# Kernel optimization log

Measured on AMD Instinct MI355X. Metric: run time of the kernel, lower is better.

## Reference

```python
import jax, jax.numpy as jnp
import numpy as np

DEPTH = 4
HEADS = 12
DIM_HEAD = 64
DIM = 768
INNER = HEADS * DIM_HEAD
MLP = 3072
K = 64
KM_ITERS = 10
B, N = 32, 196


def setup_inputs() -> dict:
    key = jax.random.key(0)
    ks = jax.random.split(key, 10)
    s = 0.02
    inp = {}
    inp["x"] = jax.random.normal(ks[0], (B, N, DIM), jnp.float32)
    inp["ln1_w"] = jnp.ones((DEPTH, DIM), jnp.float32)
    inp["ln1_b"] = jnp.zeros((DEPTH, DIM), jnp.float32)
    inp["wq"] = jax.random.normal(ks[1], (DEPTH, DIM, INNER), jnp.float32) * s
    inp["wk"] = jax.random.normal(ks[2], (DEPTH, DIM, INNER), jnp.float32) * s
    inp["wv"] = jax.random.normal(ks[3], (DEPTH, DIM, INNER), jnp.float32) * s
    inp["wo"] = jax.random.normal(ks[4], (DEPTH, INNER, DIM), jnp.float32) * s
    inp["bo"] = jnp.zeros((DEPTH, DIM), jnp.float32)
    inp["ln2_w"] = jnp.ones((DEPTH, DIM), jnp.float32)
    inp["ln2_b"] = jnp.zeros((DEPTH, DIM), jnp.float32)
    inp["w1"] = jax.random.normal(ks[5], (DEPTH, DIM, MLP), jnp.float32) * s
    inp["b1"] = jnp.zeros((DEPTH, MLP), jnp.float32)
    inp["w2"] = jax.random.normal(ks[6], (DEPTH, MLP, DIM), jnp.float32) * s
    inp["b2"] = jnp.zeros((DEPTH, DIM), jnp.float32)
    inp["ct_w"] = jax.random.normal(ks[7], (DIM, DIM), jnp.float32) * s
    inp["ct_b"] = jnp.zeros((DIM,), jnp.float32)
    return inp


def _layernorm(x, w, b, eps=1e-5):
    m = x.mean(-1, keepdims=True)
    v = jnp.mean((x - m) ** 2, -1, keepdims=True)
    return (x - m) * jax.lax.rsqrt(v + eps) * w + b


def _assign(points, centers):
    # squared distances [N, K] via expansion; argmin per point
    d = (jnp.sum(points ** 2, -1, keepdims=True)
         - 2.0 * points @ centers.T
         + jnp.sum(centers ** 2, -1))
    return jnp.argmin(d, axis=-1)


def _kmeans(points, k=K, iters=KM_ITERS):
    # Lloyd's algorithm, deterministic init = first k points
    centers0 = points[:k]

    def step(i, centers):
        labels = _assign(points, centers)
        sums = jax.ops.segment_sum(points, labels, num_segments=k)
        cnts = jax.ops.segment_sum(jnp.ones((points.shape[0],), points.dtype), labels, num_segments=k)
        new_c = sums / jnp.maximum(cnts, 1.0)[:, None]
        return jnp.where(cnts[:, None] > 0, new_c, centers)

    centers = jax.lax.fori_loop(0, iters, step, centers0)
    labels = _assign(points, centers)
    return centers, labels


def reference(x, ln1_w, ln1_b, wq, wk, wv, wo, bo, ln2_w, ln2_b, w1, b1, w2, b2, ct_w, ct_b):
    b, n, dim = x.shape
    scale = DIM_HEAD ** -0.5
    for d in range(DEPTH):
        h = _layernorm(x, ln1_w[d], ln1_b[d])
        q = (h @ wq[d]).reshape(b, n, HEADS, DIM_HEAD)
        k = (h @ wk[d]).reshape(b, n, HEADS, DIM_HEAD)
        v = (h @ wv[d]).reshape(b, n, HEADS, DIM_HEAD)
        attn = jnp.einsum('bqhd,bkhd->bhqk', q, k) * scale
        attn = jax.nn.softmax(attn, axis=-1)
        o = jnp.einsum('bhqk,bkhd->bqhd', attn, v).reshape(b, n, INNER)
        x = x + (o @ wo[d] + bo[d])
        h = _layernorm(x, ln2_w[d], ln2_b[d])
        x = x + (jax.nn.gelu(h @ w1[d] + b1[d], approximate=False) @ w2[d] + b2[d])
    # KMeans is done on detached features in the original (sklearn on cpu numpy)
    pts = jax.lax.stop_gradient(x.reshape(-1, dim))
    centers, labels = _kmeans(pts)
    clustered = centers[labels].reshape(b, n, dim)
    return clustered @ ct_w + ct_b
```

## Files before the change

kernel.cpp:

```cpp
#include <hip/hip_runtime.h>
#include <math.h>

#define M_TOK 6272
#define DIM   768
#define NHEAD 12
#define DHEAD 64
#define MLPD  3072
#define KC    64
#define S768  (768 * 768)

typedef __attribute__((ext_vector_type(8))) short bfrag8;
typedef __attribute__((ext_vector_type(4))) float floatx4;
typedef unsigned short ushort_t;

static __device__ __forceinline__ unsigned short bf16_rne(float x) {
    unsigned int u = __float_as_uint(x);
    unsigned int r = u + 0x7FFFu + ((u >> 16) & 1u);
    return (unsigned short)(r >> 16);
}

static __device__ __forceinline__ void split1(float v, unsigned short& hi, unsigned short& lo) {
    hi = bf16_rne(v);
    float hif = __uint_as_float((unsigned int)hi << 16);
    lo = bf16_rne(v - hif);
}

static __device__ __forceinline__ void split8_store(
    const float* v, unsigned short* hdst, unsigned short* ldst)
{
    bfrag8 vh, vl;
    #pragma unroll
    for (int j = 0; j < 8; ++j) {
        unsigned short hi, lo;
        split1(v[j], hi, lo);
        vh[j] = (short)hi;
        vl[j] = (short)lo;
    }
    *(bfrag8*)hdst = vh;
    *(bfrag8*)ldst = vl;
}

static __device__ __forceinline__ float block_reduce_sum(float s) {
    __shared__ float r[4];
    #pragma unroll
    for (int off = 32; off > 0; off >>= 1) s += __shfl_down(s, off);
    int lane = threadIdx.x & 63, wave = threadIdx.x >> 6;
    if (lane == 0) r[wave] = s;
    __syncthreads();
    if (threadIdx.x == 0) r[0] = r[0] + r[1] + r[2] + r[3];
    __syncthreads();
    s = r[0];
    __syncthreads();
    return s;
}

__global__ __launch_bounds__(256) void ln_split_kernel(
    const float* __restrict__ x, const float* __restrict__ w,
    const float* __restrict__ b, ushort_t* __restrict__ hh,
    ushort_t* __restrict__ hl)
{
    int row = blockIdx.x;
    const float* xr = x + (size_t)row * DIM;
    int t = threadIdx.x;
    float v0 = xr[t], v1 = xr[t + 256], v2 = xr[t + 512];
    float mean = block_reduce_sum(v0 + v1 + v2) * (1.f / 768.f);
    float d0 = v0 - mean, d1 = v1 - mean, d2 = v2 - mean;
    float var = block_reduce_sum(d0 * d0 + d1 * d1 + d2 * d2) * (1.f / 768.f);
    float rstd = rsqrtf(var + 1e-5f);
    size_t base = (size_t)row * DIM;
    float h0 = d0 * rstd * w[t]       + b[t];
    float h1 = d1 * rstd * w[t + 256] + b[t + 256];
    float h2 = d2 * rstd * w[t + 512] + b[t + 512];
    unsigned short hi, lo;
    split1(h0, hi, lo); hh[base + t]       = hi; hl[base + t]       = lo;
    split1(h1, hi, lo); hh[base + t + 256] = hi; hl[base + t + 256] = lo;
    split1(h2, hi, lo); hh[base + t + 512] = hi; hl[base + t + 512] = lo;
}

__global__ __launch_bounds__(256) void rownorm2_kernel(
    const float* __restrict__ X, float* __restrict__ out)
{
    int row = blockIdx.x;
    const float* xr = X + (size_t)row * DIM;
    int t = threadIdx.x;
    float v0 = xr[t], v1 = xr[t + 256], v2 = xr[t + 512];
    float s = block_reduce_sum(v0 * v0 + v1 * v1 + v2 * v2);
    if (t == 0) out[row] = s;
}

__global__ __launch_bounds__(256) void wsplitT_kernel(
    const float* __restrict__ W0, const float* __restrict__ W1,
    const float* __restrict__ W2, ushort_t* __restrict__ out, int K, int N)
{
    __shared__ float tile[32][33];
    const float* W = (blockIdx.z == 0) ? W0 : (blockIdx.z == 1) ? W1 : W2;
    ushort_t* oh = out + (size_t)blockIdx.z * 2 * K * N;
    ushort_t* ol = oh + (size_t)K * N;
    int kt = blockIdx.x * 32, nt = blockIdx.y * 32;
    int r = threadIdx.x >> 5, c = threadIdx.x & 31;
    #pragma unroll
    for (int i = 0; i < 4; ++i)
        tile[r + i * 8][c] = W[(size_t)(kt + r + i * 8) * N + nt + c];
    __syncthreads();
    #pragma unroll
    for (int i = 0; i < 4; ++i) {
        unsigned short hi, lo;
        split1(tile[c][r + i * 8], hi, lo);
        size_t idx = (size_t)(nt + r + i * 8) * K + kt + c;
        oh[idx] = hi; ol[idx] = lo;
    }
}


static __device__ __forceinline__ void gemm_ab_body(
    const ushort_t* __restrict__ Ah, const ushort_t* __restrict__ Al,
    const ushort_t* __restrict__ BhT, const ushort_t* __restrict__ BlT,
    const float* __restrict__ bias, const float* __restrict__ resid,
    float* __restrict__ C, int N, int K)
{
    __shared__ __align__(16) unsigned short AhL[4096];
    __shared__ __align__(16) unsigned short AlL[4096];
    __shared__ __align__(16) unsigned short BhL[4096];
    __shared__ __align__(16) unsigned short BlL[4096];

    const int tid = threadIdx.x;
    const int bm = blockIdx.y * 128, bn = blockIdx.x * 128;
    const int wave = tid >> 6, lane = tid & 63;
    const int wm = (wave >> 1) * 64, wn = (wave & 1) * 64;
    const int lrow = lane & 15, quad = lane >> 4;

    const int sm  = (tid >> 5) * 16 + 2 * (tid & 7);
    const int skq = (tid >> 3) & 3;
    const size_t arow = (size_t)(bm + sm) * K + skq * 8;
    const size_t brow = (size_t)(bn + sm) * K + skq * 8;

    floatx4 acc[4][4];
    #pragma unroll
    for (int i = 0; i < 4; ++i)
        #pragma unroll
        for (int j = 0; j < 4; ++j) acc[i][j] = floatx4{0.f, 0.f, 0.f, 0.f};

    for (int kt = 0; kt < K; kt += 32) {
        bfrag8 a0h = *(const bfrag8*)(Ah + arow + kt);
        bfrag8 a1h = *(const bfrag8*)(Ah + arow + K + kt);
        bfrag8 a0l = *(const bfrag8*)(Al + arow + kt);
        bfrag8 a1l = *(const bfrag8*)(Al + arow + K + kt);
        bfrag8 b0h = *(const bfrag8*)(BhT + brow + kt);
        bfrag8 b1h = *(const bfrag8*)(BhT + brow + K + kt);
        bfrag8 b0l = *(const bfrag8*)(BlT + brow + kt);
        bfrag8 b1l = *(const bfrag8*)(BlT + brow + K + kt);
        __syncthreads();
        *(bfrag8*)&AhL[16 * tid] = a0h;  *(bfrag8*)&AhL[16 * tid + 8] = a1h;
        *(bfrag8*)&AlL[16 * tid] = a0l;  *(bfrag8*)&AlL[16 * tid + 8] = a1l;
        *(bfrag8*)&BhL[16 * tid] = b0h;  *(bfrag8*)&BhL[16 * tid + 8] = b1h;
        *(bfrag8*)&BlL[16 * tid] = b0l;  *(bfrag8*)&BlL[16 * tid + 8] = b1l;
        __syncthreads();

        bfrag8 afh[4], afl[4], bfh[4], bfl[4];
        #pragma unroll
        for (int mt = 0; mt < 4; ++mt) {
            int base = (((wm >> 4) + mt) * 4 + quad) * 128 + lrow * 8;
            afh[mt] = *(const bfrag8*)&AhL[base];
            afl[mt] = *(const bfrag8*)&AlL[base];
        }
        #pragma unroll
        for (int nt = 0; nt < 4; ++nt) {
            int base = (((wn >> 4) + nt) * 4 + quad) * 128 + lrow * 8;
            bfh[nt] = *(const bfrag8*)&BhL[base];
            bfl[nt] = *(const bfrag8*)&BlL[base];
        }
        #pragma unroll
        for (int mt = 0; mt < 4; ++mt)
            #pragma unroll
            for (int nt = 0; nt < 4; ++nt) {
                acc[mt][nt] = __builtin_amdgcn_mfma_f32_16x16x32_bf16(
                    afh[mt], bfh[nt], acc[mt][nt], 0, 0, 0);
                acc[mt][nt] = __builtin_amdgcn_mfma_f32_16x16x32_bf16(
                    afh[mt], bfl[nt], acc[mt][nt], 0, 0, 0);
                acc[mt][nt] = __builtin_amdgcn_mfma_f32_16x16x32_bf16(
                    afl[mt], bfh[nt], acc[mt][nt], 0, 0, 0);
            }
    }

    #pragma unroll
    for (int mt = 0; mt < 4; ++mt)
        #pragma unroll
        for (int r = 0; r < 4; ++r) {
            int row = bm + wm + mt * 16 + quad * 4 + r;
            #pragma unroll
            for (int nt = 0; nt < 4; ++nt) {
                int col = bn + wn + nt * 16 + lrow;
                float v = acc[mt][nt][r];
                if (bias)  v += bias[col];
                if (resid) v += resid[(size_t)row * N + col];
                C[(size_t)row * N + col] = v;
            }
        }
}

__global__ __launch_bounds__(256) void gemm_ab_kernel(
    const ushort_t* __restrict__ Ah, const ushort_t* __restrict__ Al,
    const ushort_t* __restrict__ BhT, const ushort_t* __restrict__ BlT,
    const float* __restrict__ bias, const float* __restrict__ resid,
    float* __restrict__ C, int N, int K)
{
    gemm_ab_body(Ah, Al, BhT, BlT, bias, resid, C, N, K);
}

__global__ __launch_bounds__(256) void gemm_qkv_ab_kernel(
    const ushort_t* __restrict__ Ah, const ushort_t* __restrict__ Al,
    const ushort_t* __restrict__ wT,
    float* __restrict__ C0, float* __restrict__ C1, float* __restrict__ C2,
    int N, int K)
{
    const ushort_t* bh = wT + (size_t)blockIdx.z * 2 * S768;
    const ushort_t* bl = bh + S768;
    float* C = (blockIdx.z == 0) ? C0 : (blockIdx.z == 1) ? C1 : C2;
    gemm_ab_body(Ah, Al, bh, bl, nullptr, nullptr, C, N, K);
}

__global__ __launch_bounds__(256) void gemm_aB32_kernel(
    const ushort_t* __restrict__ Ah, const ushort_t* __restrict__ Al,
    const float* __restrict__ B, const float* __restrict__ bias,
    const float* __restrict__ resid, float* __restrict__ C,
    ushort_t* __restrict__ Ch, ushort_t* __restrict__ Cl,
    int N, int K, int act)
{
    __shared__ __align__(16) unsigned short AhL[4096];
    __shared__ __align__(16) unsigned short AlL[4096];
    __shared__ __align__(16) unsigned short BhL[4096];
    __shared__ __align__(16) unsigned short BlL[4096];

    const int tid = threadIdx.x;
    const int bm = blockIdx.y * 128, bn = blockIdx.x * 128;
    const int wave = tid >> 6, lane = tid & 63;
    const int wm = (wave >> 1) * 64, wn = (wave & 1) * 64;
    const int lrow = lane & 15, quad = lane >> 4;

    const int sm  = (tid >> 5) * 16 + 2 * (tid & 7);
    const int skq = (tid >> 3) & 3;
    const size_t arow = (size_t)(bm + sm) * K + skq * 8;
    const float* Bbase = B + (size_t)(skq * 8) * N + bn + sm;

    floatx4 acc[4][4];
    #pragma unroll
    for (int i = 0; i < 4; ++i)
        #pragma unroll
        for (int j = 0; j < 4; ++j) acc[i][j] = floatx4{0.f, 0.f, 0.f, 0.f};

    for (int kt = 0; kt < K; kt += 32) {
        bfrag8 a0h = *(const bfrag8*)(Ah + arow + kt);
        bfrag8 a1h = *(const bfrag8*)(Ah + arow + K + kt);
        bfrag8 a0l = *(const bfrag8*)(Al + arow + kt);
        bfrag8 a1l = *(const bfrag8*)(Al + arow + K + kt);
        float2 bv[8];
        #pragma unroll
        for (int j = 0; j < 8; ++j)
            bv[j] = *(const float2*)(Bbase + (size_t)(kt + j) * N);

        __syncthreads();
        *(bfrag8*)&AhL[16 * tid] = a0h;  *(bfrag8*)&AhL[16 * tid + 8] = a1h;
        *(bfrag8*)&AlL[16 * tid] = a0l;  *(bfrag8*)&AlL[16 * tid + 8] = a1l;
        {
            float b0v[8] = {bv[0].x, bv[1].x, bv[2].x, bv[3].x,
                            bv[4].x, bv[5].x, bv[6].x, bv[7].x};
            float b1v[8] = {bv[0].y, bv[1].y, bv[2].y, bv[3].y,
                            bv[4].y, bv[5].y, bv[6].y, bv[7].y};
            split8_store(b0v, &BhL[16 * tid], &BlL[16 * tid]);
            split8_store(b1v, &BhL[16 * tid + 8], &BlL[16 * tid + 8]);
        }
        __syncthreads();

        bfrag8 afh[4], afl[4], bfh[4], bfl[4];
        #pragma unroll
        for (int mt = 0; mt < 4; ++mt) {
            int base = (((wm >> 4) + mt) * 4 + quad) * 128 + lrow * 8;
            afh[mt] = *(const bfrag8*)&AhL[base];
            afl[mt] = *(const bfrag8*)&AlL[base];
        }
        #pragma unroll
        for (int nt = 0; nt < 4; ++nt) {
            int base = (((wn >> 4) + nt) * 4 + quad) * 128 + lrow * 8;
            bfh[nt] = *(const bfrag8*)&BhL[base];
            bfl[nt] = *(const bfrag8*)&BlL[base];
        }
        #pragma unroll
        for (int mt = 0; mt < 4; ++mt)
            #pragma unroll
            for (int nt = 0; nt < 4; ++nt) {
                acc[mt][nt] = __builtin_amdgcn_mfma_f32_16x16x32_bf16(
                    afh[mt], bfh[nt], acc[mt][nt], 0, 0, 0);
                acc[mt][nt] = __builtin_amdgcn_mfma_f32_16x16x32_bf16(
                    afh[mt], bfl[nt], acc[mt][nt], 0, 0, 0);
                acc[mt][nt] = __builtin_amdgcn_mfma_f32_16x16x32_bf16(
                    afl[mt], bfh[nt], acc[mt][nt], 0, 0, 0);
            }
    }

    #pragma unroll
    for (int mt = 0; mt < 4; ++mt)
        #pragma unroll
        for (int r = 0; r < 4; ++r) {
            int row = bm + wm + mt * 16 + quad * 4 + r;
            #pragma unroll
            for (int nt = 0; nt < 4; ++nt) {
                int col = bn + wn + nt * 16 + lrow;
                float v = acc[mt][nt][r];
                if (bias) v += bias[col];
                if (act)  v = 0.5f * v * (1.f + erff(v * 0.70710678118654752f));
                size_t idx = (size_t)row * N + col;
                if (Ch) {
                    unsigned short hi, lo;
                    split1(v, hi, lo);
                    Ch[idx] = hi; Cl[idx] = lo;
                } else {
                    if (resid) v += resid[idx];
                    C[idx] = v;
                }
            }
        }
}

static __device__ __forceinline__ void gemm_body(
    const float* __restrict__ A, const float* __restrict__ B,
    const float* __restrict__ bias, const float* __restrict__ resid,
    float* __restrict__ C, int M, int N, int K, int act)
{
    __shared__ float As[16][128];
    __shared__ float Bs[16][64];
    const int bm = blockIdx.y * 128;
    const int bn = blockIdx.x * 64;
    const int tid = threadIdx.x;
    const int tx = tid & 15;
    const int ty = tid >> 4;
    float acc[8][4];
    #pragma unroll
    for (int i = 0; i < 8; ++i)
        #pragma unroll
        for (int j = 0; j < 4; ++j) acc[i][j] = 0.f;

    const int a_row = tid >> 1;
    const int a_kp  = (tid & 1) * 8;
    const int b_k   = tid >> 4;
    const int b_c   = (tid & 15) * 4;

    for (int k0 = 0; k0 < K; k0 += 16) {
        int grow = bm + a_row;
        float4 a0, a1;
        if (grow < M) {
            const float* ap = A + (size_t)grow * K + (k0 + a_kp);
            a0 = *(const float4*)ap;
            a1 = *(const float4*)(ap + 4);
        } else {
            a0 = make_float4(0.f, 0.f, 0.f, 0.f); a1 = a0;
        }
        float4 bvv = *(const float4*)(B + (size_t)(k0 + b_k) * N + (bn + b_c));
        __syncthreads();
        As[a_kp + 0][a_row] = a0.x; As[a_kp + 1][a_row] = a0.y;
        As[a_kp + 2][a_row] = a0.z; As[a_kp + 3][a_row] = a0.w;
        As[a_kp + 4][a_row] = a1.x; As[a_kp + 5][a_row] = a1.y;
        As[a_kp + 6][a_row] = a1.z; As[a_kp + 7][a_row] = a1.w;
        *(float4*)&Bs[b_k][b_c] = bvv;
        __syncthreads();
        #pragma unroll
        for (int kk = 0; kk < 16; ++kk) {
            float4 af0 = *(const float4*)&As[kk][ty * 8];
            float4 af1 = *(const float4*)&As[kk][ty * 8 + 4];
            float4 bf  = *(const float4*)&Bs[kk][tx * 4];
            float a_[8] = {af0.x, af0.y, af0.z, af0.w, af1.x, af1.y, af1.z, af1.w};
            float b_[4] = {bf.x, bf.y, bf.z, bf.w};
            #pragma unroll
            for (int i = 0; i < 8; ++i)
                #pragma unroll
                for (int j = 0; j < 4; ++j)
                    acc[i][j] = fmaf(a_[i], b_[j], acc[i][j]);
        }
    }
    #pragma unroll
    for (int i = 0; i < 8; ++i) {
        int row = bm + ty * 8 + i;
        if (row < M) {
            #pragma unroll
            for (int j = 0; j < 4; ++j) {
                int col = bn + tx * 4 + j;
                float v = acc[i][j];
                if (bias)  v += bias[col];
                if (act)   v = 0.5f * v * (1.f + erff(v * 0.70710678118654752f));
                if (resid) v += resid[(size_t)row * N + col];
                C[(size_t)row * N + col] = v;
            }
        }
    }
}

__global__ __launch_bounds__(256) void gemm_kernel(
    const float* __restrict__ A, const float* __restrict__ B,
    const float* __restrict__ bias, const float* __restrict__ resid,
    float* __restrict__ C, int M, int N, int K, int act)
{
    gemm_body(A, B, bias, resid, C, M, N, K, act);
}

__global__ __launch_bounds__(256) void attn_kernel(
    const float* __restrict__ q, const float* __restrict__ k,
    const float* __restrict__ v, ushort_t* __restrict__ oh,
    ushort_t* __restrict__ ol)
{
    __shared__ float Ks[196][65];
    int qh = blockIdx.x;
    int h  = blockIdx.y;
    int b  = blockIdx.z;
    const size_t bbase = (size_t)b * 196 * DIM + (size_t)h * DHEAD;
    for (int e = threadIdx.x; e < 196 * 64; e += 256) {
        int n = e >> 6, d = e & 63;
        Ks[n][d] = k[bbase + (size_t)n * DIM + d];
    }
    __syncthreads();
    int wave = threadIdx.x >> 6, lane = threadIdx.x & 63;
    const float scale = 0.125f;
    for (int l = wave; l < 98; l += 4) {
        int qi = qh * 98 + l;
        float qv = q[bbase + (size_t)qi * DIM + lane];
        float s0 = 0.f, s1 = 0.f, s2 = 0.f, s3 = 0.f;
        #pragma unroll 8
        for (int d = 0; d < 64; ++d) {
            float qd = __shfl(qv, d);
            s0 = fmaf(qd, Ks[lane][d], s0);
            s1 = fmaf(qd, Ks[lane + 64][d], s1);
            s2 = fmaf(qd, Ks[lane + 128][d], s2);
            if (lane < 4) s3 = fmaf(qd, Ks[lane + 192][d], s3);
        }
        s0 *= scale; s1 *= scale; s2 *= scale; s3 *= scale;
        float m = fmaxf(fmaxf(s0, s1), s2);
        if (lane < 4) m = fmaxf(m, s3);
        #pragma unroll
        for (int off = 32; off > 0; off >>= 1) m = fmaxf(m, __shfl_xor(m, off));
        float e0 = expf(s0 - m), e1 = expf(s1 - m), e2 = expf(s2 - m);
        float e3 = (lane < 4) ? expf(s3 - m) : 0.f;
        float lsum = e0 + e1 + e2 + e3;
        #pragma unroll
        for (int off = 32; off > 0; off >>= 1) lsum += __shfl_xor(lsum, off);
        float inv = 1.f / lsum;
        float p0 = e0 * inv, p1 = e1 * inv, p2 = e2 * inv, p3 = e3 * inv;
        const float* vb = v + bbase + lane;
        float o0 = 0.f, o1 = 0.f, o2 = 0.f, o3 = 0.f;
        #pragma unroll 8
        for (int j = 0; j < 64; ++j) {
            o0 = fmaf(__shfl(p0, j), vb[(size_t)j * DIM], o0);
            o1 = fmaf(__shfl(p1, j), vb[(size_t)(j + 64) * DIM], o1);
            o2 = fmaf(__shfl(p2, j), vb[(size_t)(j + 128) * DIM], o2);
        }
        #pragma unroll
        for (int j = 0; j < 4; ++j)
            o3 = fmaf(__shfl(p3, j), vb[(size_t)(j + 192) * DIM], o3);
        float ov = (o0 + o1) + (o2 + o3);
        unsigned short hi, lo;
        split1(ov, hi, lo);
        oh[bbase + (size_t)qi * DIM + lane] = hi;
        ol[bbase + (size_t)qi * DIM + lane] = lo;
    }
}

__global__ __launch_bounds__(256) void transpose_ct(
    const float* __restrict__ C, float* __restrict__ CT)
{
    int i = blockIdx.x * 256 + threadIdx.x;
    if (i < DIM * KC) {
        int d = i / KC, c = i % KC;
        CT[i] = C[(size_t)c * DIM + d];
    }
}

__global__ __launch_bounds__(256) void assign_kernel(
    const float* __restrict__ P, const float* __restrict__ CT,
    const float* __restrict__ cn2, const float* __restrict__ pn2,
    int* __restrict__ labels)
{
    __shared__ float cts[256 * KC];
    int wave = threadIdx.x >> 6, lane = threadIdx.x & 63;
    int p = blockIdx.x * 4 + wave;
    float acc = 0.f;
    for (int ch = 0; ch < 3; ++ch) {
        __syncthreads();
        for (int e = threadIdx.x; e < 256 * KC / 4; e += 256)
            ((float4*)cts)[e] = ((const float4*)(CT + (size_t)ch * 256 * KC))[e];
        __syncthreads();
        const float* pr = P + (size_t)p * DIM + ch * 256;
        float a0 = 0.f, a1 = 0.f, a2 = 0.f, a3 = 0.f;
        #pragma unroll 4
        for (int kk = 0; kk < 256; kk += 4) {
            a0 = fmaf(pr[kk],     cts[(kk)     * KC + lane], a0);
            a1 = fmaf(pr[kk + 1], cts[(kk + 1) * KC + lane], a1);
            a2 = fmaf(pr[kk + 2], cts[(kk + 2) * KC + lane], a2);
            a3 = fmaf(pr[kk + 3], cts[(kk + 3) * KC + lane], a3);
        }
        acc += (a0 + a1) + (a2 + a3);
    }
    float dist = (pn2[p] - 2.f * acc) + cn2[lane];
    int idx = lane;
    #pragma unroll
    for (int off = 32; off > 0; off >>= 1) {
        float d2 = __shfl_xor(dist, off);
        int   i2 = __shfl_xor(idx, off);
        if (d2 < dist || (d2 == dist && i2 < idx)) { dist = d2; idx = i2; }
    }
    if (lane == 0) labels[p] = idx;
}

__global__ __launch_bounds__(256) void order_kernel(
    const int* __restrict__ labels, int* __restrict__ cnt,
    int* __restrict__ off, int* __restrict__ order)
{
    __shared__ int labs[M_TOK];
    __shared__ int hist[4][KC];
    __shared__ int wstart[4][KC];
    int tid = threadIdx.x;
    for (int p = tid; p < M_TOK; p += 256) labs[p] = labels[p];
    int wave = tid >> 6, lane = tid & 63;
    __syncthreads();
    const int base = wave * (M_TOK / 4);
    int h = 0;
    for (int i = 0; i < M_TOK / 4; ++i) h += (labs[base + i] == lane);
    hist[wave][lane] = h;
    __syncthreads();
    if (tid == 0) {
        int run = 0;
        for (int c = 0; c < KC; ++c) {
            int h0 = hist[0][c], h1 = hist[1][c], h2 = hist[2][c], h3 = hist[3][c];
            cnt[c] = h0 + h1 + h2 + h3;
            off[c] = run;
            wstart[0][c] = run;
            wstart[1][c] = run + h0;
            wstart[2][c] = run + h0 + h1;
            wstart[3][c] = run + h0 + h1 + h2;
            run += h0 + h1 + h2 + h3;
        }
    }
    __syncthreads();
    int pos = wstart[wave][lane];
    for (int i = 0; i < M_TOK / 4; ++i) {
        if (labs[base + i] == lane) order[pos++] = base + i;
    }
}

__global__ __launch_bounds__(768) void update_gather_kernel(
    const float* __restrict__ P, const int* __restrict__ order,
    const int* __restrict__ cnt, const int* __restrict__ off,
    const float* __restrict__ cin, float* __restrict__ cout)
{
    __shared__ int rows[M_TOK];
    int c = blockIdx.x;
    int n = cnt[c], o = off[c];
    int d = threadIdx.x;
    for (int i = d; i < n; i += 768) rows[i] = order[o + i];
    __syncthreads();
    float a0 = 0.f, a1 = 0.f, a2 = 0.f, a3 = 0.f;
    int i = 0;
    for (; i + 4 <= n; i += 4) {
        a0 += P[(size_t)rows[i]     * DIM + d];
        a1 += P[(size_t)rows[i + 1] * DIM + d];
        a2 += P[(size_t)rows[i + 2] * DIM + d];
        a3 += P[(size_t)rows[i + 3] * DIM + d];
    }
    for (; i < n; ++i) a0 += P[(size_t)rows[i] * DIM + d];
    float s = (a0 + a1) + (a2 + a3);
    cout[(size_t)c * DIM + d] = (n > 0) ? (s / (float)n) : cin[(size_t)c * DIM + d];
}

__global__ __launch_bounds__(256) void gather_kernel(
    const float* __restrict__ cproj, const int* __restrict__ labels,
    float* __restrict__ out)
{
    int i = blockIdx.x * 256 + threadIdx.x;
    int p = i / DIM, d = i - p * DIM;
    out[i] = cproj[(size_t)labels[p] * DIM + d];
}

extern "C" void kernel_launch(void* const* d_in, const int* in_sizes, int n_in,
                              void* d_out, int out_size, void* d_ws, size_t ws_size,
                              hipStream_t stream)
{
    const float* x    = (const float*)d_in[0];
    const float* ln1w = (const float*)d_in[1];
    const float* ln1b = (const float*)d_in[2];
    const float* wq   = (const float*)d_in[3];
    const float* wk   = (const float*)d_in[4];
    const float* wv   = (const float*)d_in[5];
    const float* wo   = (const float*)d_in[6];
    const float* bo   = (const float*)d_in[7];
    const float* ln2w = (const float*)d_in[8];
    const float* ln2b = (const float*)d_in[9];
    const float* w1   = (const float*)d_in[10];
    const float* b1   = (const float*)d_in[11];
    const float* w2   = (const float*)d_in[12];
    const float* b2   = (const float*)d_in[13];
    const float* ctw  = (const float*)d_in[14];
    const float* ctb  = (const float*)d_in[15];

    const size_t M768 = (size_t)M_TOK * DIM;
    float* ws    = (float*)d_ws;
    float* xbuf  = ws;
    float* qbuf  = xbuf + M768;
    float* kbuf  = qbuf + M768;
    float* vbuf  = kbuf + M768;
    float* obuf  = vbuf + M768;
    float* cA    = obuf + M768;
    float* cB    = cA + (size_t)KC * DIM;
    float* CT    = cB + (size_t)KC * DIM;
    float* cproj = CT + (size_t)KC * DIM;
    float* cn2   = cproj + (size_t)KC * DIM;
    float* pn2   = cn2 + KC;
    int*  labels = (int*)(pn2 + M_TOK);
    int*  cnt    = labels + M_TOK;
    int*  coff   = cnt + KC;
    int*  order  = coff + KC;

    ushort_t* hh    = (ushort_t*)d_out;
    ushort_t* hl    = hh + M768;
    ushort_t* woT   = (ushort_t*)d_out;
    ushort_t* wqkvT = (ushort_t*)obuf;
    ushort_t* oh    = (ushort_t*)obuf;
    ushort_t* ol    = oh + M768;
    ushort_t* m1h   = (ushort_t*)qbuf;
    ushort_t* m1l   = m1h + (size_t)M_TOK * MLPD;

    hipMemcpyAsync(xbuf, x, M768 * sizeof(float), hipMemcpyDeviceToDevice, stream);

    dim3 blk(256);
    dim3 gN768(DIM / 128, M_TOK / 128);
    dim3 gN3072(MLPD / 128, M_TOK / 128);
    dim3 gqkv(DIM / 128, M_TOK / 128, 3);
    dim3 gsplit3(DIM / 32, DIM / 32, 3);
    dim3 gsplit1(DIM / 32, DIM / 32, 1);

    for (int d = 0; d < 4; ++d) {
        size_t w768 = (size_t)d * DIM * DIM;
        ln_split_kernel<<<M_TOK, blk, 0, stream>>>(xbuf, ln1w + d * DIM, ln1b + d * DIM, hh, hl);
        wsplitT_kernel<<<gsplit3, blk, 0, stream>>>(wq + w768, wk + w768, wv + w768,
                                                    wqkvT, DIM, DIM);
        gemm_qkv_ab_kernel<<<gqkv, blk, 0, stream>>>(hh, hl, wqkvT, qbuf, kbuf, vbuf, DIM, DIM);
        attn_kernel<<<dim3(2, NHEAD, 32), blk, 0, stream>>>(qbuf, kbuf, vbuf, oh, ol);
        wsplitT_kernel<<<gsplit1, blk, 0, stream>>>(wo + w768, wo + w768, wo + w768,
                                                    woT, DIM, DIM);
        gemm_ab_kernel<<<gN768, blk, 0, stream>>>(oh, ol, woT, woT + S768,
                                                  bo + d * DIM, xbuf, xbuf, DIM, DIM);
        ln_split_kernel<<<M_TOK, blk, 0, stream>>>(xbuf, ln2w + d * DIM, ln2b + d * DIM, hh, hl);
        gemm_aB32_kernel<<<gN3072, blk, 0, stream>>>(hh, hl, w1 + (size_t)d * DIM * MLPD,
                                                     b1 + d * MLPD, nullptr, nullptr,
                                                     m1h, m1l, MLPD, DIM, 1);
        gemm_aB32_kernel<<<gN768, blk, 0, stream>>>(m1h, m1l, w2 + (size_t)d * MLPD * DIM,
                                                    b2 + d * DIM, xbuf, xbuf,
                                                    nullptr, nullptr, DIM, MLPD, 0);
    }

    rownorm2_kernel<<<M_TOK, blk, 0, stream>>>(xbuf, pn2);
    hipMemcpyAsync(cA, xbuf, (size_t)KC * DIM * sizeof(float),
                   hipMemcpyDeviceToDevice, stream);
    float* cin = cA; float* cout = cB;
    for (int it = 0; it < 10; ++it) {
        rownorm2_kernel<<<KC, blk, 0, stream>>>(cin, cn2);
        transpose_ct<<<(KC * DIM + 255) / 256, blk, 0, stream>>>(cin, CT);
        assign_kernel<<<M_TOK / 4, blk, 0, stream>>>(xbuf, CT, cn2, pn2, labels);
        order_kernel<<<1, blk, 0, stream>>>(labels, cnt, coff, order);
        update_gather_kernel<<<KC, dim3(768), 0, stream>>>(xbuf, order, cnt, coff, cin, cout);
        float* t = cin; cin = cout; cout = t;
    }
    rownorm2_kernel<<<KC, blk, 0, stream>>>(cin, cn2);
    transpose_ct<<<(KC * DIM + 255) / 256, blk, 0, stream>>>(cin, CT);
    assign_kernel<<<M_TOK / 4, blk, 0, stream>>>(xbuf, CT, cn2, pn2, labels);

    gemm_kernel<<<dim3(DIM / 64, 1), blk, 0, stream>>>(cin, ctw, ctb, nullptr, cproj,
                                                       KC, DIM, DIM, 0);
    gather_kernel<<<(M_TOK * DIM) / 256, blk, 0, stream>>>(cproj, labels, (float*)d_out);
}
```

Before: 6.085 ms.

## Rewrite attention with split-bf16 MFMA and emit split Q/K from QKV GEMM

Replaces the scalar FMA attention kernel with one that computes QK^T and PV on bf16 MFMA units, using a hi/lo split with three products to keep near-fp32 accuracy. The QKV GEMM epilogue now writes Q and K directly as hi/lo bf16 pairs, so attention loads ready-made MFMA fragments. Softmax runs in registers and the probabilities are staged in LDS, while V is split and transposed per tile in LDS. This removes the scalar dot-product and shuffle-heavy loops, at the cost of extra LDS traffic, syncthreads inside the PV loop, and wasted work on padding to 208/224 tokens.

```diff
diff --git a/kernel.cpp b/kernel.cpp
--- a/kernel.cpp
+++ b/kernel.cpp
@@ -116,7 +116,8 @@
     const ushort_t* __restrict__ Ah, const ushort_t* __restrict__ Al,
     const ushort_t* __restrict__ BhT, const ushort_t* __restrict__ BlT,
     const float* __restrict__ bias, const float* __restrict__ resid,
-    float* __restrict__ C, int N, int K)
+    float* __restrict__ C, ushort_t* __restrict__ Ch, ushort_t* __restrict__ Cl,
+    int N, int K)
 {
     __shared__ __align__(16) unsigned short AhL[4096];
     __shared__ __align__(16) unsigned short AlL[4096];
@@ -192,8 +193,15 @@
                 int col = bn + wn + nt * 16 + lrow;
                 float v = acc[mt][nt][r];
                 if (bias)  v += bias[col];
-                if (resid) v += resid[(size_t)row * N + col];
-                C[(size_t)row * N + col] = v;
+                size_t idx = (size_t)row * N + col;
+                if (Ch) {
+                    unsigned short hi, lo;
+                    split1(v, hi, lo);
+                    Ch[idx] = hi; Cl[idx] = lo;
+                } else {
+                    if (resid) v += resid[idx];
+                    C[idx] = v;
+                }
             }
         }
 }
@@ -204,19 +212,24 @@
     const float* __restrict__ bias, const float* __restrict__ resid,
     float* __restrict__ C, int N, int K)
 {
-    gemm_ab_body(Ah, Al, BhT, BlT, bias, resid, C, N, K);
+    gemm_ab_body(Ah, Al, BhT, BlT, bias, resid, C, nullptr, nullptr, N, K);
 }
 
 __global__ __launch_bounds__(256) void gemm_qkv_ab_kernel(
     const ushort_t* __restrict__ Ah, const ushort_t* __restrict__ Al,
     const ushort_t* __restrict__ wT,
-    float* __restrict__ C0, float* __restrict__ C1, float* __restrict__ C2,
-    int N, int K)
+    ushort_t* __restrict__ q_h, ushort_t* __restrict__ q_l,
+    ushort_t* __restrict__ k_h, ushort_t* __restrict__ k_l,
+    float* __restrict__ vf, int N, int K)
 {
     const ushort_t* bh = wT + (size_t)blockIdx.z * 2 * S768;
     const ushort_t* bl = bh + S768;
-    float* C = (blockIdx.z == 0) ? C0 : (blockIdx.z == 1) ? C1 : C2;
-    gemm_ab_body(Ah, Al, bh, bl, nullptr, nullptr, C, N, K);
+    if (blockIdx.z == 0)
+        gemm_ab_body(Ah, Al, bh, bl, nullptr, nullptr, nullptr, q_h, q_l, N, K);
+    else if (blockIdx.z == 1)
+        gemm_ab_body(Ah, Al, bh, bl, nullptr, nullptr, nullptr, k_h, k_l, N, K);
+    else
+        gemm_ab_body(Ah, Al, bh, bl, nullptr, nullptr, vf, nullptr, nullptr, N, K);
 }
 
 __global__ __launch_bounds__(256) void gemm_aB32_kernel(
@@ -401,64 +414,145 @@
     gemm_body(A, B, bias, resid, C, M, N, K, act);
 }
 
-__global__ __launch_bounds__(256) void attn_kernel(
-    const float* __restrict__ q, const float* __restrict__ k,
+__global__ __launch_bounds__(256) void attn_mfma_kernel(
+    const ushort_t* __restrict__ qh, const ushort_t* __restrict__ ql,
+    const ushort_t* __restrict__ kh, const ushort_t* __restrict__ kl,
     const float* __restrict__ v, ushort_t* __restrict__ oh,
     ushort_t* __restrict__ ol)
 {
-    __shared__ float Ks[196][65];
-    int qh = blockIdx.x;
-    int h  = blockIdx.y;
-    int b  = blockIdx.z;
-    const size_t bbase = (size_t)b * 196 * DIM + (size_t)h * DHEAD;
-    for (int e = threadIdx.x; e < 196 * 64; e += 256) {
-        int n = e >> 6, d = e & 63;
-        Ks[n][d] = k[bbase + (size_t)n * DIM + d];
-    }
-    __syncthreads();
-    int wave = threadIdx.x >> 6, lane = threadIdx.x & 63;
+    __shared__ __align__(16) ushort_t Ph[64 * 224];
+    __shared__ __align__(16) ushort_t Pl[64 * 224];
+    __shared__ __align__(16) ushort_t VTh[32 * 32];
+    __shared__ __align__(16) ushort_t VTl[32 * 32];
+
+    const int tid = threadIdx.x;
+    const int w = tid >> 6, lane = tid & 63;
+    const int lrow = lane & 15, quad = lane >> 4;
+    const int hbase = (int)blockIdx.y * DHEAD;
+    const int b = blockIdx.z;
+    const int mt = blockIdx.x * 4 + w;
+    const size_t tok0 = (size_t)b * 196;
+
+    int qrow = mt * 16 + lrow; if (qrow > 195) qrow = 195;
+    const size_t qoff = (tok0 + qrow) * DIM + hbase + quad * 8;
+    bfrag8 qfh0 = *(const bfrag8*)(qh + qoff);
+    bfrag8 qfh1 = *(const bfrag8*)(qh + qoff + 32);
+    bfrag8 qfl0 = *(const bfrag8*)(ql + qoff);
+    bfrag8 qfl1 = *(const bfrag8*)(ql + qoff + 32);
+
+    floatx4 sacc[13];
+    #pragma unroll
+    for (int nt = 0; nt < 13; ++nt) {
+        int krow = nt * 16 + lrow; if (krow > 195) krow = 195;
+        const size_t koff = (tok0 + krow) * DIM + hbase + quad * 8;
+        bfrag8 kfh0 = *(const bfrag8*)(kh + koff);
+        bfrag8 kfh1 = *(const bfrag8*)(kh + koff + 32);
+        bfrag8 kfl0 = *(const bfrag8*)(kl + koff);
+        bfrag8 kfl1 = *(const bfrag8*)(kl + koff + 32);
+        floatx4 a = floatx4{0.f, 0.f, 0.f, 0.f};
+        a = __builtin_amdgcn_mfma_f32_16x16x32_bf16(qfh0, kfh0, a, 0, 0, 0);
+        a = __builtin_amdgcn_mfma_f32_16x16x32_bf16(qfh0, kfl0, a, 0, 0, 0);
+        a = __builtin_amdgcn_mfma_f32_16x16x32_bf16(qfl0, kfh0, a, 0, 0, 0);
+        a = __builtin_amdgcn_mfma_f32_16x16x32_bf16(qfh1, kfh1, a, 0, 0, 0);
+        a = __builtin_amdgcn_mfma_f32_16x16x32_bf16(qfh1, kfl1, a, 0, 0, 0);
+        a = __builtin_amdgcn_mfma_f32_16x16x32_bf16(qfl1, kfh1, a, 0, 0, 0);
+        sacc[nt] = a;
+    }
+
     const float scale = 0.125f;
-    for (int l = wave; l < 98; l += 4) {
-        int qi = qh * 98 + l;
-        float qv = q[bbase + (size_t)qi * DIM + lane];
-        float s0 = 0.f, s1 = 0.f, s2 = 0.f, s3 = 0.f;
-        #pragma unroll 8
-        for (int d = 0; d < 64; ++d) {
-            float qd = __shfl(qv, d);
-            s0 = fmaf(qd, Ks[lane][d], s0);
-            s1 = fmaf(qd, Ks[lane + 64][d], s1);
-            s2 = fmaf(qd, Ks[lane + 128][d], s2);
-            if (lane < 4) s3 = fmaf(qd, Ks[lane + 192][d], s3);
-        }
-        s0 *= scale; s1 *= scale; s2 *= scale; s3 *= scale;
-        float m = fmaxf(fmaxf(s0, s1), s2);
-        if (lane < 4) m = fmaxf(m, s3);
-        #pragma unroll
-        for (int off = 32; off > 0; off >>= 1) m = fmaxf(m, __shfl_xor(m, off));
-        float e0 = expf(s0 - m), e1 = expf(s1 - m), e2 = expf(s2 - m);
-        float e3 = (lane < 4) ? expf(s3 - m) : 0.f;
-        float lsum = e0 + e1 + e2 + e3;
-        #pragma unroll
-        for (int off = 32; off > 0; off >>= 1) lsum += __shfl_xor(lsum, off);
-        float inv = 1.f / lsum;
-        float p0 = e0 * inv, p1 = e1 * inv, p2 = e2 * inv, p3 = e3 * inv;
-        const float* vb = v + bbase + lane;
-        float o0 = 0.f, o1 = 0.f, o2 = 0.f, o3 = 0.f;
-        #pragma unroll 8
-        for (int j = 0; j < 64; ++j) {
-            o0 = fmaf(__shfl(p0, j), vb[(size_t)j * DIM], o0);
-            o1 = fmaf(__shfl(p1, j), vb[(size_t)(j + 64) * DIM], o1);
-            o2 = fmaf(__shfl(p2, j), vb[(size_t)(j + 128) * DIM], o2);
-        }
-        #pragma unroll
-        for (int j = 0; j < 4; ++j)
-            o3 = fmaf(__shfl(p3, j), vb[(size_t)(j + 192) * DIM], o3);
-        float ov = (o0 + o1) + (o2 + o3);
-        unsigned short hi, lo;
-        split1(ov, hi, lo);
-        oh[bbase + (size_t)qi * DIM + lane] = hi;
-        ol[bbase + (size_t)qi * DIM + lane] = lo;
-    }
+    #pragma unroll
+    for (int r = 0; r < 4; ++r) {
+        float m = -3.0e38f;
+        #pragma unroll
+        for (int nt = 0; nt < 13; ++nt) {
+            float s = sacc[nt][r] * scale;
+            if (nt == 12 && lrow >= 4) s = -1.0e30f;
+            sacc[nt][r] = s;
+            m = fmaxf(m, s);
+        }
+        m = fmaxf(m, __shfl_xor(m, 1));
+        m = fmaxf(m, __shfl_xor(m, 2));
+        m = fmaxf(m, __shfl_xor(m, 4));
+        m = fmaxf(m, __shfl_xor(m, 8));
+        float l = 0.f;
+        #pragma unroll
+        for (int nt = 0; nt < 13; ++nt) {
+            float e = expf(sacc[nt][r] - m);
+            sacc[nt][r] = e;
+            l += e;
+        }
+        l += __shfl_xor(l, 1);
+        l += __shfl_xor(l, 2);
+        l += __shfl_xor(l, 4);
+        l += __shfl_xor(l, 8);
+        float inv = 1.f / l;
+        int prow = w * 16 + quad * 4 + r;
+        #pragma unroll
+        for (int nt = 0; nt < 13; ++nt) {
+            unsigned short hi, lo;
+            split1(sacc[nt][r] * inv, hi, lo);
+            int pidx = prow * 224 + nt * 16 + lrow;
+            Ph[pidx] = hi; Pl[pidx] = lo;
+        }
+    }
+    for (int i = lane; i < 16 * 28; i += 64) {
+        int rr = i / 28, cc = 196 + i % 28;
+        int pidx = (w * 16 + rr) * 224 + cc;
+        Ph[pidx] = 0; Pl[pidx] = 0;
+    }
+
+    floatx4 oacc[4];
+    #pragma unroll
+    for (int i = 0; i < 4; ++i) oacc[i] = floatx4{0.f, 0.f, 0.f, 0.f};
+
+    for (int ks = 0; ks < 7; ++ks) {
+        #pragma unroll
+        for (int dh = 0; dh < 2; ++dh) {
+            __syncthreads();
+            {
+                int kloc = tid >> 3;
+                int dloc = (tid & 7) * 4;
+                int vrow = ks * 32 + kloc;
+                float4 vv = make_float4(0.f, 0.f, 0.f, 0.f);
+                if (vrow < 196)
+                    vv = *(const float4*)(v + (tok0 + vrow) * DIM + hbase + dh * 32 + dloc);
+                float vs[4] = {vv.x, vv.y, vv.z, vv.w};
+                #pragma unroll
+                for (int i = 0; i < 4; ++i) {
+                    unsigned short hi, lo;
+                    split1(vs[i], hi, lo);
+                    VTh[(dloc + i) * 32 + kloc] = hi;
+                    VTl[(dloc + i) * 32 + kloc] = lo;
+                }
+            }
+            __syncthreads();
+            bfrag8 pah = *(const bfrag8*)&Ph[(w * 16 + lrow) * 224 + ks * 32 + quad * 8];
+            bfrag8 pal = *(const bfrag8*)&Pl[(w * 16 + lrow) * 224 + ks * 32 + quad * 8];
+            #pragma unroll
+            for (int ntl = 0; ntl < 2; ++ntl) {
+                bfrag8 vbh = *(const bfrag8*)&VTh[(ntl * 16 + lrow) * 32 + quad * 8];
+                bfrag8 vbl = *(const bfrag8*)&VTl[(ntl * 16 + lrow) * 32 + quad * 8];
+                int nt = dh * 2 + ntl;
+                oacc[nt] = __builtin_amdgcn_mfma_f32_16x16x32_bf16(pah, vbh, oacc[nt], 0, 0, 0);
+                oacc[nt] = __builtin_amdgcn_mfma_f32_16x16x32_bf16(pah, vbl, oacc[nt], 0, 0, 0);
+                oacc[nt] = __builtin_amdgcn_mfma_f32_16x16x32_bf16(pal, vbh, oacc[nt], 0, 0, 0);
+            }
+        }
+    }
+
+    #pragma unroll
+    for (int nt = 0; nt < 4; ++nt)
+        #pragma unroll
+        for (int r = 0; r < 4; ++r) {
+            int row = mt * 16 + quad * 4 + r;
+            if (row < 196) {
+                int d = nt * 16 + lrow;
+                unsigned short hi, lo;
+                split1(oacc[nt][r], hi, lo);
+                size_t off = (tok0 + row) * DIM + hbase + d;
+                oh[off] = hi; ol[off] = lo;
+            }
+        }
 }
 
 __global__ __launch_bounds__(256) void transpose_ct(
@@ -619,6 +713,10 @@
     ushort_t* hl    = hh + M768;
     ushort_t* woT   = (ushort_t*)d_out;
     ushort_t* wqkvT = (ushort_t*)obuf;
+    ushort_t* q_h   = (ushort_t*)qbuf;
+    ushort_t* q_l   = q_h + M768;
+    ushort_t* k_h   = (ushort_t*)kbuf;
+    ushort_t* k_l   = k_h + M768;
     ushort_t* oh    = (ushort_t*)obuf;
     ushort_t* ol    = oh + M768;
     ushort_t* m1h   = (ushort_t*)qbuf;
@@ -632,14 +730,16 @@
     dim3 gqkv(DIM / 128, M_TOK / 128, 3);
     dim3 gsplit3(DIM / 32, DIM / 32, 3);
     dim3 gsplit1(DIM / 32, DIM / 32, 1);
+    dim3 gattn(4, NHEAD, 32);
 
     for (int d = 0; d < 4; ++d) {
         size_t w768 = (size_t)d * DIM * DIM;
         ln_split_kernel<<<M_TOK, blk, 0, stream>>>(xbuf, ln1w + d * DIM, ln1b + d * DIM, hh, hl);
         wsplitT_kernel<<<gsplit3, blk, 0, stream>>>(wq + w768, wk + w768, wv + w768,
                                                     wqkvT, DIM, DIM);
-        gemm_qkv_ab_kernel<<<gqkv, blk, 0, stream>>>(hh, hl, wqkvT, qbuf, kbuf, vbuf, DIM, DIM);
-        attn_kernel<<<dim3(2, NHEAD, 32), blk, 0, stream>>>(qbuf, kbuf, vbuf, oh, ol);
+        gemm_qkv_ab_kernel<<<gqkv, blk, 0, stream>>>(hh, hl, wqkvT,
+                                                     q_h, q_l, k_h, k_l, vbuf, DIM, DIM);
+        attn_mfma_kernel<<<gattn, blk, 0, stream>>>(q_h, q_l, k_h, k_l, vbuf, oh, ol);
         wsplitT_kernel<<<gsplit1, blk, 0, stream>>>(wo + w768, wo + w768, wo + w768,
                                                     woT, DIM, DIM);
         gemm_ab_kernel<<<gN768, blk, 0, stream>>>(oh, ol, woT, woT + S768,
```

Result: faster. 5.155 ms (-15.3%).
